# Kernel tuning notes

Hardware: AMD Instinct MI355X
Metric: run time of the kernel (lower is better)

Reference implementation:

```python
import jax
import jax.numpy as jnp
import numpy as np
from jax import lax

SEQ_LEN = 512
INPUT_DIM = 256
NUM_HIDDEN = 1024
NUM_CLASSES = 10
BATCH = 256


def setup_inputs() -> dict:
    key = jax.random.key(0)
    k1, k2, k3, k4 = jax.random.split(key, 4)
    x = jax.random.normal(k1, (BATCH, SEQ_LEN, INPUT_DIM), dtype=jnp.float32)
    # orthogonal-ish init scale ~1; plain normal is fine for a numeric reference
    w_hx = jax.random.normal(k2, (NUM_HIDDEN, INPUT_DIM), dtype=jnp.float32) * 0.02
    w_hh = jax.random.normal(k3, (NUM_HIDDEN, NUM_HIDDEN), dtype=jnp.float32) * 0.02
    b_h = jnp.zeros((NUM_HIDDEN, 1), dtype=jnp.float32)
    w_ph = jax.random.normal(k4, (NUM_CLASSES, NUM_HIDDEN), dtype=jnp.float32) * 0.0001
    b_p = jnp.zeros((NUM_CLASSES, 1), dtype=jnp.float32)
    return {"x": x, "w_hx": w_hx, "w_hh": w_hh, "b_h": b_h, "w_ph": w_ph, "b_p": b_p}


def reference(x, w_hx, w_hh, b_h, w_ph, b_p):
    # x: [B, S, I]; hidden state kept as [H, B] matching torch's column-major layout
    B = x.shape[0]
    H = w_hh.shape[0]
    h0 = jnp.zeros((H, B), dtype=x.dtype)  # h_init is a fixed zero buffer
    xs = jnp.swapaxes(x, 0, 1)  # [S, B, I]

    def step(h, xt):
        # xt: [B, I] -> w_hx @ xt.T : [H, B]
        h_new = jnp.tanh(w_hx @ xt.T + w_hh @ h + b_h)
        return h_new, None

    h_final, _ = lax.scan(step, h0, xs)
    p = w_ph @ h_final + b_p  # [C, B]
    return p.T  # [B, C]
```

## Files before the change

### kernel.cpp

```cpp
#include <hip/hip_runtime.h>

#define SEQ  512
#define IDIM 256
#define HD   1024
#define BT   256
#define NCLS 10

#define GR    8
#define GB    16
#define NWG   (GR*GB)
#define TPB   512
#define KKH   32
#define KKX   8
#define NSLOT 4
#define SENT  0x7F80

typedef __attribute__((ext_vector_type(8))) short short8;
typedef __attribute__((ext_vector_type(4))) float f32x4;
typedef __attribute__((ext_vector_type(4))) unsigned short us4;
typedef __attribute__((ext_vector_type(4))) int i32x4;

__device__ unsigned short g_h[NSLOT][GB][KKH*64*8];
__device__ float g_hfinal[BT][HD];
__device__ unsigned g_bar, g_done_all;

__device__ __forceinline__ unsigned short f2bf(float f){
    unsigned int u = __builtin_bit_cast(unsigned int, f);
    u += 0x7fffu + ((u >> 16) & 1u);
    return (unsigned short)(u >> 16);
}
__device__ __forceinline__ float fast_tanh(float v){
    float e = __expf(2.0f * v);
    return 1.0f - 2.0f / (e + 1.0f);
}
__device__ __forceinline__ void sys_st64(unsigned short* p, unsigned long long v){
    __hip_atomic_store((unsigned long long*)p, v, __ATOMIC_RELAXED, __HIP_MEMORY_SCOPE_SYSTEM);
}

__global__
__attribute__((amdgpu_flat_work_group_size(TPB, TPB), amdgpu_waves_per_eu(2, 2)))
void rnn_main(
    const float* __restrict__ x, const float* __restrict__ w_hx,
    const float* __restrict__ w_hh, const float* __restrict__ b_h)
{
    __shared__ unsigned short sX[8*KKX*64*8];
    __shared__ unsigned short sB2[2][KKH*64*8];

    const int tid = threadIdx.x;
    const int wg  = blockIdx.x;
    const int gbg = wg & (GB-1);
    const int gr  = wg >> 4;
    const int r0  = gr * 128;
    const int b0  = gbg * 16;
    const int l   = tid & 63;
    const int w   = tid >> 6;
    const int rw  = r0 + w*16;
    const int row = rw + (l & 15);
    const int ko  = (l >> 4) << 3;

    i32x4 wa[KKH];
    #pragma unroll
    for (int kk = 0; kk < KKH; ++kk){
        f32x4 v0 = *(const f32x4*)(w_hh + (size_t)row*HD + kk*32 + ko);
        f32x4 v1 = *(const f32x4*)(w_hh + (size_t)row*HD + kk*32 + ko + 4);
        us4 lo = { f2bf(v0[0]), f2bf(v0[1]), f2bf(v0[2]), f2bf(v0[3]) };
        us4 hi = { f2bf(v1[0]), f2bf(v1[1]), f2bf(v1[2]), f2bf(v1[3]) };
        unsigned long long a = __builtin_bit_cast(unsigned long long, lo);
        unsigned long long b = __builtin_bit_cast(unsigned long long, hi);
        i32x4 q;
        q[0] = (int)(a & 0xffffffffu); q[1] = (int)(a >> 32);
        q[2] = (int)(b & 0xffffffffu); q[3] = (int)(b >> 32);
        wa[kk] = q;
    }
    #pragma unroll
    for (int kk = 0; kk < KKH; ++kk)
        asm volatile("" : "+v"(wa[kk]));

    #pragma unroll
    for (int xk = 0; xk < KKX; ++xk){
        f32x4 v0 = *(const f32x4*)(w_hx + (size_t)row*IDIM + xk*32 + ko);
        f32x4 v1 = *(const f32x4*)(w_hx + (size_t)row*IDIM + xk*32 + ko + 4);
        short8 a;
        a[0]=(short)f2bf(v0[0]); a[1]=(short)f2bf(v0[1]);
        a[2]=(short)f2bf(v0[2]); a[3]=(short)f2bf(v0[3]);
        a[4]=(short)f2bf(v1[0]); a[5]=(short)f2bf(v1[1]);
        a[6]=(short)f2bf(v1[2]); a[7]=(short)f2bf(v1[3]);
        *(short8*)&sX[(size_t)((w*KKX + xk)*64 + l)*8] = a;
    }

    const f32x4 bias = *(const f32x4*)(b_h + rw + ((l >> 4) << 2));
    const float* xlane = x + (size_t)(b0 + (l & 15))*(SEQ*IDIM) + ko;

    const int rloc  = w*16 + ((l >> 4) << 2);
    const int kkd   = gr*4 + (rloc >> 5);
    const int lnp   = (l & 15) | (((rloc >> 3) & 3) << 4);
    const int sboff = kkd*512 + lnp*8 + (rloc & 7);
    us4 hw_prev = {0, 0, 0, 0};

    sys_st64(&g_h[0][gbg][sboff], 0ull);
    {
        int sv = SENT;
        #pragma unroll
        for (int s = 1; s < NSLOT; ++s){
            unsigned short* p = &g_h[s][gbg][sboff];
            asm volatile("global_store_short %0, %1, off sc0 sc1" :: "v"(p), "v"(sv) : "memory");
        }
    }
    asm volatile("s_waitcnt vmcnt(0)" ::: "memory");
    __syncthreads();

    if (tid == 0){
        __hip_atomic_fetch_add(&g_bar, 1u, __ATOMIC_ACQ_REL, __HIP_MEMORY_SCOPE_SYSTEM);
        int guard = 0;
        while (__hip_atomic_load(&g_bar, __ATOMIC_ACQUIRE, __HIP_MEMORY_SCOPE_SYSTEM) < NWG
               && ++guard < (1 << 22)) { }
    }
    __syncthreads();

    auto xpart = [&](const float* xp) -> f32x4 {
        f32x4 a = bias;
        #pragma unroll
        for (int xk = 0; xk < KKX; ++xk){
            f32x4 v0 = *(const f32x4*)(xp + xk*32);
            f32x4 v1 = *(const f32x4*)(xp + xk*32 + 4);
            short8 bx;
            bx[0]=(short)f2bf(v0[0]); bx[1]=(short)f2bf(v0[1]);
            bx[2]=(short)f2bf(v0[2]); bx[3]=(short)f2bf(v0[3]);
            bx[4]=(short)f2bf(v1[0]); bx[5]=(short)f2bf(v1[1]);
            bx[6]=(short)f2bf(v1[2]); bx[7]=(short)f2bf(v1[3]);
            short8 aw = *(const short8*)&sX[(size_t)((w*KKX + xk)*64 + l)*8];
            a = __builtin_amdgcn_mfma_f32_16x16x32_bf16(aw, bx, a, 0, 0, 0);
        }
        return a;
    };
    f32x4 accX = xpart(xlane);

    for (int t = 0; t < SEQ; ++t){
        const int slot  = t & 3;
        const int nslot = (t + 1) & 3;
        const int pslot = (t + 3) & 3;
        unsigned short* sB = &sB2[t & 1][0];

        *(us4*)&sB[sboff] = hw_prev;
        if (w != gr){
            const unsigned short* base = &g_h[slot][gbg][(size_t)(w*4)*512 + l*8];
            i32x4 v0, v1, v2, v3;
            int guard = 0;
            for (;;){
                asm volatile(
                    "global_load_dwordx4 %0, %4, off sc0 sc1\n\t"
                    "global_load_dwordx4 %1, %4, off offset:1024 sc0 sc1\n\t"
                    "global_load_dwordx4 %2, %4, off offset:2048 sc0 sc1\n\t"
                    "global_load_dwordx4 %3, %4, off offset:3072 sc0 sc1"
                    : "=&v"(v0), "=&v"(v1), "=&v"(v2), "=&v"(v3)
                    : "v"(base));
                asm volatile("s_waitcnt vmcnt(0)" ::: "memory");
                bool ok = ((v0[0] & 0xFFFF) != SENT) && ((v0[2] & 0xFFFF) != SENT)
                       && ((v1[0] & 0xFFFF) != SENT) && ((v1[2] & 0xFFFF) != SENT)
                       && ((v2[0] & 0xFFFF) != SENT) && ((v2[2] & 0xFFFF) != SENT)
                       && ((v3[0] & 0xFFFF) != SENT) && ((v3[2] & 0xFFFF) != SENT);
                if (__all(ok)) break;
                if (++guard > (1 << 20)) break;
            }
            *(i32x4*)&sB[(size_t)(w*4+0)*512 + l*8] = v0;
            *(i32x4*)&sB[(size_t)(w*4+1)*512 + l*8] = v1;
            *(i32x4*)&sB[(size_t)(w*4+2)*512 + l*8] = v2;
            *(i32x4*)&sB[(size_t)(w*4+3)*512 + l*8] = v3;
        } else {
            asm volatile("s_waitcnt vmcnt(0)" ::: "memory");
        }
        __syncthreads();

        {
            int sv = SENT;
            unsigned short* p = &g_h[pslot][gbg][sboff];
            asm volatile("global_store_short %0, %1, off sc0 sc1" :: "v"(p), "v"(sv) : "memory");
        }

        f32x4 acc = accX;
        #pragma unroll
        for (int kk = 0; kk < KKH; ++kk){
            short8 b = *(const short8*)&sB[(size_t)(kk*64 + l)*8];
            acc = __builtin_amdgcn_mfma_f32_16x16x32_bf16(
                      __builtin_bit_cast(short8, wa[kk]), b, acc, 0, 0, 0);
        }
        float h0 = fast_tanh(acc[0]);
        float h1 = fast_tanh(acc[1]);
        float h2 = fast_tanh(acc[2]);
        float h3 = fast_tanh(acc[3]);

        if (t < SEQ-1){
            us4 hw = { f2bf(h0), f2bf(h1), f2bf(h2), f2bf(h3) };
            sys_st64(&g_h[nslot][gbg][sboff],
                     __builtin_bit_cast(unsigned long long, hw));
            hw_prev = hw;
            accX = xpart(xlane + (size_t)(t+1)*IDIM);
        } else {
            f32x4 hf = {h0, h1, h2, h3};
            *(f32x4*)&g_hfinal[b0 + (l & 15)][r0 + rloc] = hf;
        }
    }

    __syncthreads();
    if (tid == 0){
        unsigned old = __hip_atomic_fetch_add(&g_done_all, 1u,
                           __ATOMIC_ACQ_REL, __HIP_MEMORY_SCOPE_SYSTEM);
        if (old == NWG - 1){
            __hip_atomic_store(&g_bar,      0u, __ATOMIC_RELAXED, __HIP_MEMORY_SCOPE_SYSTEM);
            __hip_atomic_store(&g_done_all, 0u, __ATOMIC_RELAXED, __HIP_MEMORY_SCOPE_SYSTEM);
        }
    }
}

__global__ __launch_bounds__(256, 1) void proj_kernel(
    const float* __restrict__ w_ph, const float* __restrict__ b_p, float* __restrict__ out)
{
    const int b   = blockIdx.x;
    const int tid = threadIdx.x;
    const int l   = tid & 63;
    const int wv  = tid >> 6;
    __shared__ float red[4];
    f32x4 hv = *(const f32x4*)(&g_hfinal[b][0] + tid*4);
    for (int c = 0; c < NCLS; ++c){
        f32x4 wvv = *(const f32x4*)(w_ph + c*HD + tid*4);
        float s = hv[0]*wvv[0] + hv[1]*wvv[1] + hv[2]*wvv[2] + hv[3]*wvv[3];
        #pragma unroll
        for (int off = 32; off; off >>= 1) s += __shfl_down(s, off, 64);
        if (l == 0) red[wv] = s;
        __syncthreads();
        if (tid == 0) out[b*NCLS + c] = red[0] + red[1] + red[2] + red[3] + b_p[c];
        __syncthreads();
    }
}

extern "C" void kernel_launch(void* const* d_in, const int* in_sizes, int n_in,
                              void* d_out, int out_size, void* d_ws, size_t ws_size,
                              hipStream_t stream) {
    const float* x    = (const float*)d_in[0];
    const float* w_hx = (const float*)d_in[1];
    const float* w_hh = (const float*)d_in[2];
    const float* b_h  = (const float*)d_in[3];
    const float* w_ph = (const float*)d_in[4];
    const float* b_p  = (const float*)d_in[5];

    void* args[] = { (void*)&x, (void*)&w_hx, (void*)&w_hh, (void*)&b_h };
    hipError_t err = hipLaunchCooperativeKernel((void*)rnn_main, dim3(NWG), dim3(TPB),
                                                args, 0, stream);
    if (err != hipSuccess) {
        rnn_main<<<dim3(NWG), dim3(TPB), 0, stream>>>(x, w_hx, w_hh, b_h);
    }
    proj_kernel<<<dim3(BT), dim3(256), 0, stream>>>(w_ph, b_p, (float*)d_out);
}
```

Before: 2.621 ms.

## Stage hidden-state publish through LDS and store it from one wave in bulk

Each wave now writes its new bf16 hidden values into a shared-memory staging buffer. After an extra workgroup barrier, the single wave that owns this row block publishes them to the global exchange slot with wide dwordx4 system-scope stores, along with vectorized sentinel resets. This replaces the many scattered 64-bit atomic stores and short sentinel stores per thread. The double-buffered LDS tile becomes single-buffered, the polling loop gains s_sleep with a smaller guard, and the x-projection moves after the publish so it overlaps the wait. The cost is a second barrier per timestep and funnelling the publish latency through one wave.

```diff
diff --git a/kernel.cpp b/kernel.cpp
--- a/kernel.cpp
+++ b/kernel.cpp
@@ -36,6 +36,12 @@
 __device__ __forceinline__ void sys_st64(unsigned short* p, unsigned long long v){
     __hip_atomic_store((unsigned long long*)p, v, __ATOMIC_RELAXED, __HIP_MEMORY_SCOPE_SYSTEM);
 }
+__device__ __forceinline__ void bar_lgkm(){
+    asm volatile("s_waitcnt lgkmcnt(0)" ::: "memory");
+    __builtin_amdgcn_sched_barrier(0);
+    __builtin_amdgcn_s_barrier();
+    __builtin_amdgcn_sched_barrier(0);
+}
 
 __global__
 __attribute__((amdgpu_flat_work_group_size(TPB, TPB), amdgpu_waves_per_eu(2, 2)))
@@ -44,7 +50,8 @@
     const float* __restrict__ w_hh, const float* __restrict__ b_h)
 {
     __shared__ unsigned short sX[8*KKX*64*8];
-    __shared__ unsigned short sB2[2][KKH*64*8];
+    __shared__ unsigned short sB[KKH*64*8];
+    __shared__ unsigned long long hbuf[512];
 
     const int tid = threadIdx.x;
     const int wg  = blockIdx.x;
@@ -95,6 +102,7 @@
     const int kkd   = gr*4 + (rloc >> 5);
     const int lnp   = (l & 15) | (((rloc >> 3) & 3) << 4);
     const int sboff = kkd*512 + lnp*8 + (rloc & 7);
+    const int loc   = sboff - gr*4*512;
     us4 hw_prev = {0, 0, 0, 0};
 
     sys_st64(&g_h[0][gbg][sboff], 0ull);
@@ -108,7 +116,6 @@
     }
     asm volatile("s_waitcnt vmcnt(0)" ::: "memory");
     __syncthreads();
-
     if (tid == 0){
         __hip_atomic_fetch_add(&g_bar, 1u, __ATOMIC_ACQ_REL, __HIP_MEMORY_SCOPE_SYSTEM);
         int guard = 0;
@@ -136,10 +143,9 @@
     f32x4 accX = xpart(xlane);
 
     for (int t = 0; t < SEQ; ++t){
-        const int slot  = t & 3;
-        const int nslot = (t + 1) & 3;
-        const int pslot = (t + 3) & 3;
-        unsigned short* sB = &sB2[t & 1][0];
+        const int slot = t & 3;
+        const int ns   = (t + 1) & 3;
+        const int ps   = (t + 3) & 3;
 
         *(us4*)&sB[sboff] = hw_prev;
         if (w != gr){
@@ -160,22 +166,15 @@
                        && ((v2[0] & 0xFFFF) != SENT) && ((v2[2] & 0xFFFF) != SENT)
                        && ((v3[0] & 0xFFFF) != SENT) && ((v3[2] & 0xFFFF) != SENT);
                 if (__all(ok)) break;
-                if (++guard > (1 << 20)) break;
+                if (++guard > (1 << 18)) break;
+                __builtin_amdgcn_s_sleep(1);
             }
             *(i32x4*)&sB[(size_t)(w*4+0)*512 + l*8] = v0;
             *(i32x4*)&sB[(size_t)(w*4+1)*512 + l*8] = v1;
             *(i32x4*)&sB[(size_t)(w*4+2)*512 + l*8] = v2;
             *(i32x4*)&sB[(size_t)(w*4+3)*512 + l*8] = v3;
-        } else {
-            asm volatile("s_waitcnt vmcnt(0)" ::: "memory");
-        }
-        __syncthreads();
-
-        {
-            int sv = SENT;
-            unsigned short* p = &g_h[pslot][gbg][sboff];
-            asm volatile("global_store_short %0, %1, off sc0 sc1" :: "v"(p), "v"(sv) : "memory");
-        }
+        }
+        bar_lgkm();
 
         f32x4 acc = accX;
         #pragma unroll
@@ -191,14 +190,38 @@
 
         if (t < SEQ-1){
             us4 hw = { f2bf(h0), f2bf(h1), f2bf(h2), f2bf(h3) };
-            sys_st64(&g_h[nslot][gbg][sboff],
-                     __builtin_bit_cast(unsigned long long, hw));
+            hbuf[loc >> 2] = __builtin_bit_cast(unsigned long long, hw);
             hw_prev = hw;
-            accX = xpart(xlane + (size_t)(t+1)*IDIM);
         } else {
             f32x4 hf = {h0, h1, h2, h3};
             *(f32x4*)&g_hfinal[b0 + (l & 15)][r0 + rloc] = hf;
         }
+        bar_lgkm();
+
+        if (w == gr && t < SEQ-1){
+            asm volatile("s_waitcnt vmcnt(8)" ::: "memory");
+            i32x4 d0 = *(i32x4*)&hbuf[(size_t)l*8 + 0];
+            i32x4 d1 = *(i32x4*)&hbuf[(size_t)l*8 + 2];
+            i32x4 d2 = *(i32x4*)&hbuf[(size_t)l*8 + 4];
+            i32x4 d3 = *(i32x4*)&hbuf[(size_t)l*8 + 6];
+            unsigned short* dd = &g_h[ns][gbg][(size_t)gr*2048 + l*32];
+            asm volatile(
+                "global_store_dwordx4 %0, %1, off sc0 sc1\n\t"
+                "global_store_dwordx4 %0, %2, off offset:16 sc0 sc1\n\t"
+                "global_store_dwordx4 %0, %3, off offset:32 sc0 sc1\n\t"
+                "global_store_dwordx4 %0, %4, off offset:48 sc0 sc1"
+                :: "v"(dd), "v"(d0), "v"(d1), "v"(d2), "v"(d3) : "memory");
+            i32x4 sv = { SENT, 0, SENT, 0 };
+            unsigned short* ds = &g_h[ps][gbg][(size_t)gr*2048 + l*32];
+            asm volatile(
+                "global_store_dwordx4 %0, %1, off sc0 sc1\n\t"
+                "global_store_dwordx4 %0, %1, off offset:16 sc0 sc1\n\t"
+                "global_store_dwordx4 %0, %1, off offset:32 sc0 sc1\n\t"
+                "global_store_dwordx4 %0, %1, off offset:48 sc0 sc1"
+                :: "v"(ds), "v"(sv) : "memory");
+        }
+        if (t < SEQ-1)
+            accX = xpart(xlane + (size_t)(t+1)*IDIM);
     }
 
     __syncthreads();
```

Result: slower. 2.909 ms (+11.0%).

## Split recurrent MFMA chain, lighten barrier, reorder stores and x loads

Applied to the files above, without the earlier changes.

Splits the 32-long dependent MFMA accumulation into four independent chains that are summed at the end, which shortens the per-step latency on the critical path. Swaps __syncthreads for an LDS-only wait plus s_barrier, so the pending sentinel store no longer forces a wait on vector memory. Moves the sentinel reset after the h publish, and issues the next step's x loads with inline asm before the h store, waiting with a partial vmcnt so the stores overlap the x projection. Risks memory-ordering subtleties with the custom waitcnt, and the shorter spin guard could time out early.

```diff
diff --git a/kernel.cpp b/kernel.cpp
--- a/kernel.cpp
+++ b/kernel.cpp
@@ -35,6 +35,12 @@
 }
 __device__ __forceinline__ void sys_st64(unsigned short* p, unsigned long long v){
     __hip_atomic_store((unsigned long long*)p, v, __ATOMIC_RELAXED, __HIP_MEMORY_SCOPE_SYSTEM);
+}
+__device__ __forceinline__ void bar_lgkm(){
+    asm volatile("s_waitcnt lgkmcnt(0)" ::: "memory");
+    __builtin_amdgcn_sched_barrier(0);
+    __builtin_amdgcn_s_barrier();
+    __builtin_amdgcn_sched_barrier(0);
 }
 
 __global__
@@ -108,7 +114,6 @@
     }
     asm volatile("s_waitcnt vmcnt(0)" ::: "memory");
     __syncthreads();
-
     if (tid == 0){
         __hip_atomic_fetch_add(&g_bar, 1u, __ATOMIC_ACQ_REL, __HIP_MEMORY_SCOPE_SYSTEM);
         int guard = 0;
@@ -117,28 +122,24 @@
     }
     __syncthreads();
 
-    auto xpart = [&](const float* xp) -> f32x4 {
-        f32x4 a = bias;
-        #pragma unroll
-        for (int xk = 0; xk < KKX; ++xk){
-            f32x4 v0 = *(const f32x4*)(xp + xk*32);
-            f32x4 v1 = *(const f32x4*)(xp + xk*32 + 4);
-            short8 bx;
-            bx[0]=(short)f2bf(v0[0]); bx[1]=(short)f2bf(v0[1]);
-            bx[2]=(short)f2bf(v0[2]); bx[3]=(short)f2bf(v0[3]);
-            bx[4]=(short)f2bf(v1[0]); bx[5]=(short)f2bf(v1[1]);
-            bx[6]=(short)f2bf(v1[2]); bx[7]=(short)f2bf(v1[3]);
-            short8 aw = *(const short8*)&sX[(size_t)((w*KKX + xk)*64 + l)*8];
-            a = __builtin_amdgcn_mfma_f32_16x16x32_bf16(aw, bx, a, 0, 0, 0);
-        }
-        return a;
-    };
-    f32x4 accX = xpart(xlane);
+    f32x4 accX = bias;
+    #pragma unroll
+    for (int xk = 0; xk < KKX; ++xk){
+        f32x4 v0 = *(const f32x4*)(xlane + xk*32);
+        f32x4 v1 = *(const f32x4*)(xlane + xk*32 + 4);
+        short8 bx;
+        bx[0]=(short)f2bf(v0[0]); bx[1]=(short)f2bf(v0[1]);
+        bx[2]=(short)f2bf(v0[2]); bx[3]=(short)f2bf(v0[3]);
+        bx[4]=(short)f2bf(v1[0]); bx[5]=(short)f2bf(v1[1]);
+        bx[6]=(short)f2bf(v1[2]); bx[7]=(short)f2bf(v1[3]);
+        short8 aw = *(const short8*)&sX[(size_t)((w*KKX + xk)*64 + l)*8];
+        accX = __builtin_amdgcn_mfma_f32_16x16x32_bf16(aw, bx, accX, 0, 0, 0);
+    }
 
     for (int t = 0; t < SEQ; ++t){
-        const int slot  = t & 3;
-        const int nslot = (t + 1) & 3;
-        const int pslot = (t + 3) & 3;
+        const int slot = t & 3;
+        const int ns   = (t + 1) & 3;
+        const int ps   = (t + 3) & 3;
         unsigned short* sB = &sB2[t & 1][0];
 
         *(us4*)&sB[sboff] = hw_prev;
@@ -160,41 +161,73 @@
                        && ((v2[0] & 0xFFFF) != SENT) && ((v2[2] & 0xFFFF) != SENT)
                        && ((v3[0] & 0xFFFF) != SENT) && ((v3[2] & 0xFFFF) != SENT);
                 if (__all(ok)) break;
-                if (++guard > (1 << 20)) break;
+                if (++guard > (1 << 18)) break;
             }
             *(i32x4*)&sB[(size_t)(w*4+0)*512 + l*8] = v0;
             *(i32x4*)&sB[(size_t)(w*4+1)*512 + l*8] = v1;
             *(i32x4*)&sB[(size_t)(w*4+2)*512 + l*8] = v2;
             *(i32x4*)&sB[(size_t)(w*4+3)*512 + l*8] = v3;
-        } else {
-            asm volatile("s_waitcnt vmcnt(0)" ::: "memory");
-        }
-        __syncthreads();
-
-        {
-            int sv = SENT;
-            unsigned short* p = &g_h[pslot][gbg][sboff];
-            asm volatile("global_store_short %0, %1, off sc0 sc1" :: "v"(p), "v"(sv) : "memory");
-        }
-
-        f32x4 acc = accX;
+        }
+        bar_lgkm();
+
+        f32x4 a0 = accX;
+        f32x4 a1 = {0.f,0.f,0.f,0.f}, a2 = {0.f,0.f,0.f,0.f}, a3 = {0.f,0.f,0.f,0.f};
         #pragma unroll
-        for (int kk = 0; kk < KKH; ++kk){
-            short8 b = *(const short8*)&sB[(size_t)(kk*64 + l)*8];
-            acc = __builtin_amdgcn_mfma_f32_16x16x32_bf16(
-                      __builtin_bit_cast(short8, wa[kk]), b, acc, 0, 0, 0);
-        }
+        for (int kk = 0; kk < KKH; kk += 4){
+            short8 b0 = *(const short8*)&sB[(size_t)((kk+0)*64 + l)*8];
+            short8 b1 = *(const short8*)&sB[(size_t)((kk+1)*64 + l)*8];
+            short8 b2 = *(const short8*)&sB[(size_t)((kk+2)*64 + l)*8];
+            short8 b3 = *(const short8*)&sB[(size_t)((kk+3)*64 + l)*8];
+            a0 = __builtin_amdgcn_mfma_f32_16x16x32_bf16(
+                     __builtin_bit_cast(short8, wa[kk+0]), b0, a0, 0, 0, 0);
+            a1 = __builtin_amdgcn_mfma_f32_16x16x32_bf16(
+                     __builtin_bit_cast(short8, wa[kk+1]), b1, a1, 0, 0, 0);
+            a2 = __builtin_amdgcn_mfma_f32_16x16x32_bf16(
+                     __builtin_bit_cast(short8, wa[kk+2]), b2, a2, 0, 0, 0);
+            a3 = __builtin_amdgcn_mfma_f32_16x16x32_bf16(
+                     __builtin_bit_cast(short8, wa[kk+3]), b3, a3, 0, 0, 0);
+        }
+        f32x4 acc = (a0 + a1) + (a2 + a3);
         float h0 = fast_tanh(acc[0]);
         float h1 = fast_tanh(acc[1]);
         float h2 = fast_tanh(acc[2]);
         float h3 = fast_tanh(acc[3]);
 
         if (t < SEQ-1){
+            const float* xp = xlane + (size_t)(t+1)*IDIM;
+            f32x4 xv0[8], xv1[8];
+            #pragma unroll
+            for (int xk = 0; xk < KKX; ++xk){
+                const float* p0 = xp + xk*32;
+                const float* p1 = xp + xk*32 + 4;
+                asm volatile("global_load_dwordx4 %0, %1, off" : "=&v"(xv0[xk]) : "v"(p0));
+                asm volatile("global_load_dwordx4 %0, %1, off" : "=&v"(xv1[xk]) : "v"(p1));
+            }
             us4 hw = { f2bf(h0), f2bf(h1), f2bf(h2), f2bf(h3) };
-            sys_st64(&g_h[nslot][gbg][sboff],
-                     __builtin_bit_cast(unsigned long long, hw));
+            unsigned long long hbits = __builtin_bit_cast(unsigned long long, hw);
+            unsigned short* hp = &g_h[ns][gbg][sboff];
+            asm volatile("global_store_dwordx2 %0, %1, off sc0 sc1" :: "v"(hp), "v"(hbits) : "memory");
             hw_prev = hw;
-            accX = xpart(xlane + (size_t)(t+1)*IDIM);
+            {
+                int sv = SENT;
+                unsigned short* sp = &g_h[ps][gbg][sboff];
+                asm volatile("global_store_short %0, %1, off sc0 sc1" :: "v"(sp), "v"(sv) : "memory");
+            }
+            asm volatile("s_waitcnt vmcnt(2)" ::: "memory");
+            __builtin_amdgcn_sched_barrier(0);
+            f32x4 aX = bias;
+            #pragma unroll
+            for (int xk = 0; xk < KKX; ++xk){
+                f32x4 v0 = xv0[xk], v1 = xv1[xk];
+                short8 bx;
+                bx[0]=(short)f2bf(v0[0]); bx[1]=(short)f2bf(v0[1]);
+                bx[2]=(short)f2bf(v0[2]); bx[3]=(short)f2bf(v0[3]);
+                bx[4]=(short)f2bf(v1[0]); bx[5]=(short)f2bf(v1[1]);
+                bx[6]=(short)f2bf(v1[2]); bx[7]=(short)f2bf(v1[3]);
+                short8 aw = *(const short8*)&sX[(size_t)((w*KKX + xk)*64 + l)*8];
+                aX = __builtin_amdgcn_mfma_f32_16x16x32_bf16(aw, bx, aX, 0, 0, 0);
+            }
+            accX = aX;
         } else {
             f32x4 hf = {h0, h1, h2, h3};
             *(f32x4*)&g_hfinal[b0 + (l & 15)][r0 + rloc] = hf;
```

After: 2.740 ms. 4.6% more time.

## Replace per-step workgroup barrier with per-wave LDS ready flags and split accumulators

Applied to the files above, without the earlier changes.

Removes the __syncthreads per timestep. Each wave now loads its own chunk of h from global memory, including the chunk for its own row group that was previously written locally, and publishes an LDS ready counter. The MFMA loop consumes chunks in wave order, spinning on each peer's flag, so compute overlaps with other waves' loads. Two accumulators break the MFMA dependency chain. The sentinel-reset store moves after the compute and the spin guard is reduced. The risks are LDS flag spin overhead and the double-buffered sB being overwritten while a slow wave still reads it, since no barrier separates steps t and t+2.

```diff
diff --git a/kernel.cpp b/kernel.cpp
--- a/kernel.cpp
+++ b/kernel.cpp
@@ -45,6 +45,7 @@
 {
     __shared__ unsigned short sX[8*KKX*64*8];
     __shared__ unsigned short sB2[2][KKH*64*8];
+    __shared__ int sready[8];
 
     const int tid = threadIdx.x;
     const int wg  = blockIdx.x;
@@ -95,7 +96,6 @@
     const int kkd   = gr*4 + (rloc >> 5);
     const int lnp   = (l & 15) | (((rloc >> 3) & 3) << 4);
     const int sboff = kkd*512 + lnp*8 + (rloc & 7);
-    us4 hw_prev = {0, 0, 0, 0};
 
     sys_st64(&g_h[0][gbg][sboff], 0ull);
     {
@@ -106,9 +106,9 @@
             asm volatile("global_store_short %0, %1, off sc0 sc1" :: "v"(p), "v"(sv) : "memory");
         }
     }
+    if (tid < 8) sready[tid] = 0;
     asm volatile("s_waitcnt vmcnt(0)" ::: "memory");
     __syncthreads();
-
     if (tid == 0){
         __hip_atomic_fetch_add(&g_bar, 1u, __ATOMIC_ACQ_REL, __HIP_MEMORY_SCOPE_SYSTEM);
         int guard = 0;
@@ -136,13 +136,12 @@
     f32x4 accX = xpart(xlane);
 
     for (int t = 0; t < SEQ; ++t){
-        const int slot  = t & 3;
-        const int nslot = (t + 1) & 3;
-        const int pslot = (t + 3) & 3;
+        const int slot = t & 3;
+        const int ns   = (t + 1) & 3;
+        const int ps   = (t + 3) & 3;
         unsigned short* sB = &sB2[t & 1][0];
 
-        *(us4*)&sB[sboff] = hw_prev;
-        if (w != gr){
+        {
             const unsigned short* base = &g_h[slot][gbg][(size_t)(w*4)*512 + l*8];
             i32x4 v0, v1, v2, v3;
             int guard = 0;
@@ -160,30 +159,43 @@
                        && ((v2[0] & 0xFFFF) != SENT) && ((v2[2] & 0xFFFF) != SENT)
                        && ((v3[0] & 0xFFFF) != SENT) && ((v3[2] & 0xFFFF) != SENT);
                 if (__all(ok)) break;
-                if (++guard > (1 << 20)) break;
+                if (++guard > (1 << 18)) break;
             }
             *(i32x4*)&sB[(size_t)(w*4+0)*512 + l*8] = v0;
             *(i32x4*)&sB[(size_t)(w*4+1)*512 + l*8] = v1;
             *(i32x4*)&sB[(size_t)(w*4+2)*512 + l*8] = v2;
             *(i32x4*)&sB[(size_t)(w*4+3)*512 + l*8] = v3;
-        } else {
-            asm volatile("s_waitcnt vmcnt(0)" ::: "memory");
-        }
-        __syncthreads();
-
-        {
-            int sv = SENT;
-            unsigned short* p = &g_h[pslot][gbg][sboff];
-            asm volatile("global_store_short %0, %1, off sc0 sc1" :: "v"(p), "v"(sv) : "memory");
-        }
-
-        f32x4 acc = accX;
-        #pragma unroll
-        for (int kk = 0; kk < KKH; ++kk){
-            short8 b = *(const short8*)&sB[(size_t)(kk*64 + l)*8];
-            acc = __builtin_amdgcn_mfma_f32_16x16x32_bf16(
-                      __builtin_bit_cast(short8, wa[kk]), b, acc, 0, 0, 0);
-        }
+            if (l == 0)
+                __hip_atomic_store(&sready[w], t + 1,
+                                   __ATOMIC_RELEASE, __HIP_MEMORY_SCOPE_WORKGROUP);
+        }
+
+        f32x4 a0 = accX, a1 = {0.f,0.f,0.f,0.f};
+        #pragma unroll
+        for (int p = 0; p < 8; ++p){
+            if (p != w){
+                int guard = 0;
+                while (__hip_atomic_load(&sready[p], __ATOMIC_RELAXED,
+                                         __HIP_MEMORY_SCOPE_WORKGROUP) < t + 1){
+                    if (++guard > (1 << 22)) break;
+                }
+                __builtin_amdgcn_fence(__ATOMIC_ACQUIRE, "workgroup");
+                __builtin_amdgcn_sched_barrier(0);
+            }
+            short8 b0 = *(const short8*)&sB[(size_t)((p*4+0)*64 + l)*8];
+            short8 b1 = *(const short8*)&sB[(size_t)((p*4+1)*64 + l)*8];
+            short8 b2 = *(const short8*)&sB[(size_t)((p*4+2)*64 + l)*8];
+            short8 b3 = *(const short8*)&sB[(size_t)((p*4+3)*64 + l)*8];
+            a0 = __builtin_amdgcn_mfma_f32_16x16x32_bf16(
+                     __builtin_bit_cast(short8, wa[p*4+0]), b0, a0, 0, 0, 0);
+            a1 = __builtin_amdgcn_mfma_f32_16x16x32_bf16(
+                     __builtin_bit_cast(short8, wa[p*4+1]), b1, a1, 0, 0, 0);
+            a0 = __builtin_amdgcn_mfma_f32_16x16x32_bf16(
+                     __builtin_bit_cast(short8, wa[p*4+2]), b2, a0, 0, 0, 0);
+            a1 = __builtin_amdgcn_mfma_f32_16x16x32_bf16(
+                     __builtin_bit_cast(short8, wa[p*4+3]), b3, a1, 0, 0, 0);
+        }
+        f32x4 acc = a0 + a1;
         float h0 = fast_tanh(acc[0]);
         float h1 = fast_tanh(acc[1]);
         float h2 = fast_tanh(acc[2]);
@@ -191,9 +203,14 @@
 
         if (t < SEQ-1){
             us4 hw = { f2bf(h0), f2bf(h1), f2bf(h2), f2bf(h3) };
-            sys_st64(&g_h[nslot][gbg][sboff],
-                     __builtin_bit_cast(unsigned long long, hw));
-            hw_prev = hw;
+            unsigned long long hbits = __builtin_bit_cast(unsigned long long, hw);
+            unsigned short* hp = &g_h[ns][gbg][sboff];
+            asm volatile("global_store_dwordx2 %0, %1, off sc0 sc1" :: "v"(hp), "v"(hbits) : "memory");
+            {
+                int sv = SENT;
+                unsigned short* sp = &g_h[ps][gbg][sboff];
+                asm volatile("global_store_short %0, %1, off sc0 sc1" :: "v"(sp), "v"(sv) : "memory");
+            }
             accX = xpart(xlane + (size_t)(t+1)*IDIM);
         } else {
             f32x4 hf = {h0, h1, h2, h3};
```

New measurement: 2.712 ms. 1.03x slower.
